# Kernel tuning notes

Hardware: AMD Instinct MI355X
Metric: run time of the kernel (lower is better)

The kernel has to match this reference:

```python
import jax, jax.numpy as jnp
import numpy as np

N_NODES = 100000
N_EDGES = 1600000
IN_CH = 128
TYPE_EMB = 32
OUT_CH = 128
N_REL = 8
N_BASES = 8
N_NTYPES = 8
FEAT = IN_CH + TYPE_EMB  # 160, RGCNConv input dim after concat


def setup_inputs() -> dict:
    key = jax.random.key(0)
    ks = jax.random.split(key, 9)
    x = jax.random.normal(ks[0], (N_NODES, IN_CH), dtype=jnp.float32)
    node_type_ids = jax.random.randint(ks[1], (N_NODES,), 0, N_NTYPES)
    edge_index = jax.random.randint(ks[2], (2, N_EDGES), 0, N_NODES)
    edge_type = jax.random.randint(ks[3], (N_EDGES,), 0, N_REL)
    emb_table = jax.random.normal(ks[4], (N_NTYPES, TYPE_EMB), dtype=jnp.float32)
    bases = jax.random.normal(ks[5], (N_BASES, FEAT, OUT_CH), dtype=jnp.float32) * (1.0 / np.sqrt(FEAT))
    comp = jax.random.normal(ks[6], (N_REL, N_BASES), dtype=jnp.float32) * (1.0 / np.sqrt(N_BASES))
    root_w = jax.random.normal(ks[7], (FEAT, OUT_CH), dtype=jnp.float32) * (1.0 / np.sqrt(FEAT))
    bias = jnp.zeros((OUT_CH,), dtype=jnp.float32)
    return {"x": x, "node_type_ids": node_type_ids, "edge_index": edge_index,
            "edge_type": edge_type, "emb_table": emb_table, "bases": bases,
            "comp": comp, "root_w": root_w, "bias": bias}


def reference(x, node_type_ids, edge_index, edge_type, emb_table, bases, comp, root_w, bias):
    N = x.shape[0]
    # node-type embedding lookup + concat
    h = jnp.concatenate([x, emb_table[node_type_ids]], axis=1)  # [N, FEAT]
    # basis decomposition: per-relation weights [R, FEAT, OUT]
    weight = jnp.einsum('rb,bio->rio', comp, bases)
    src, dst = edge_index[0], edge_index[1]
    h_src = h[src]  # [E, FEAT] -- dominant gather
    # root/self transform + bias
    out = h @ root_w + bias
    # PyG RGCNConv default aggr='mean': per-relation mean over incoming edges, summed across relations
    for r in range(weight.shape[0]):
        m = (edge_type == r).astype(h.dtype)  # [E]
        s = jax.ops.segment_sum(h_src * m[:, None], dst, num_segments=N)  # [N, FEAT]
        c = jax.ops.segment_sum(m, dst, num_segments=N)                    # [N]
        mean_r = s / jnp.maximum(c, 1.0)[:, None]
        out = out + mean_r @ weight[r]
    # dropout is identity in eval mode
    return jax.nn.relu(out)
```

## Files before the change

kernel.cpp:

```cpp
#include <hip/hip_runtime.h>

#define NN 100000
#define NE 1600000
#define INC 128
#define TE 32
#define OC 128
#define NR 8
#define NBASES 8
#define FT 160
#define KP 168
#define KW 160
#define TN 32
#define NBKT 3125
#define NCH 256
#define EPB 6250
#define CAP 896

typedef float f32x4 __attribute__((ext_vector_type(4)));
typedef float f32x2 __attribute__((ext_vector_type(2)));
typedef __bf16 bf16x8 __attribute__((ext_vector_type(8)));

__device__ __forceinline__ unsigned f2bf1(float f) {
    unsigned u = __float_as_uint(f);
    return (u + 0x7fffu + ((u >> 16) & 1u)) >> 16;
}

__device__ __forceinline__ float bflo(unsigned u) { return __uint_as_float(u << 16); }
__device__ __forceinline__ float bfhi(unsigned u) { return __uint_as_float(u & 0xFFFF0000u); }

__device__ __forceinline__ unsigned cvtpk(float a, float b) {
    unsigned r;
    asm("v_cvt_pk_bf16_f32 %0, %1, %2" : "=v"(r) : "v"(a), "v"(b));
    return r;
}

__device__ __forceinline__ int bscan_excl(int v, int* tmp) {
    int tid = threadIdx.x;
    tmp[tid] = v; __syncthreads();
#pragma unroll
    for (int d = 1; d < 256; d <<= 1) {
        int t = (tid >= d) ? tmp[tid - d] : 0;
        __syncthreads();
        tmp[tid] += t;
        __syncthreads();
    }
    return tmp[tid] - v;
}

__global__ __launch_bounds__(256) void k_prep(
    const float* __restrict__ x, const int* __restrict__ nt,
    const float* __restrict__ emb, const float* __restrict__ comp,
    const float* __restrict__ bases, const float* __restrict__ rootw,
    const int* __restrict__ ei,
    unsigned short* __restrict__ h, unsigned short* __restrict__ Wt,
    int* __restrict__ ghist, int* __restrict__ total) {
    __shared__ int hist[NBKT];
    int tid = threadIdx.x;
    int b = blockIdx.x;
    if (b < NCH) {
        for (int j = tid; j < NBKT; j += 256) hist[j] = 0;
        __syncthreads();
        int e0 = b * EPB;
#pragma unroll
        for (int kk = 0; kk < 28; kk += 4) {
            int dv[4];
#pragma unroll
            for (int u = 0; u < 4; u++) {
                int i = (kk + u) * 256 + tid;
                dv[u] = (i < EPB) ? ei[NE + e0 + i] : -1;
            }
#pragma unroll
            for (int u = 0; u < 4; u++)
                if (dv[u] >= 0) atomicAdd(&hist[dv[u] >> 5], 1);
        }
        __syncthreads();
        int* g = ghist + (size_t)b * NBKT;
        for (int j = tid; j < NBKT; j += 256) {
            int v = hist[j];
            g[j] = v;
            if (v) atomicAdd(&total[j], v);
        }
        return;
    }
    int idx = (b - NCH) * 256 + tid;
    if (idx < 9 * 128 * KW) {
        int ridx = idx / (128 * KW);
        int rem  = idx % (128 * KW);
        int o = rem / KW;
        int k = rem % KW;
        float v = 0.f;
        if (k < 128) {
            if (ridx < NR) {
#pragma unroll
                for (int bb = 0; bb < NBASES; bb++)
                    v += comp[ridx * NBASES + bb] * bases[(bb * FT + k) * OC + o];
            } else {
                v = rootw[k * OC + o];
            }
        } else if (k < 136) {
            int t = k - 128;
            if (ridx < NR) {
#pragma unroll
                for (int bb = 0; bb < NBASES; bb++) {
                    float cb = comp[ridx * NBASES + bb], s2 = 0.f;
                    for (int k2 = 0; k2 < TE; k2++)
                        s2 += emb[t * TE + k2] * bases[(bb * FT + 128 + k2) * OC + o];
                    v += cb * s2;
                }
            } else {
                for (int k2 = 0; k2 < TE; k2++)
                    v += emb[t * TE + k2] * rootw[(128 + k2) * OC + o];
            }
        }
        Wt[idx] = (unsigned short)f2bf1(v);
    }
    if (idx < NN * 16) {
        int n = idx / 16, c = idx % 16;
        const float* p = x + (size_t)n * INC + c * 8;
        f32x4 v0 = *(const f32x4*)p, v1 = *(const f32x4*)(p + 4);
        uint4 o;
        o.x = f2bf1(v0.x) | (f2bf1(v0.y) << 16);
        o.y = f2bf1(v0.z) | (f2bf1(v0.w) << 16);
        o.z = f2bf1(v1.x) | (f2bf1(v1.y) << 16);
        o.w = f2bf1(v1.z) | (f2bf1(v1.w) << 16);
        *(uint4*)(h + (size_t)n * INC + c * 8) = o;
    }
}

__global__ __launch_bounds__(256) void k_scanoff(const int* __restrict__ total,
                                                 int* __restrict__ ghist,
                                                 int* __restrict__ bstart) {
    __shared__ int tot[NBKT];
    __shared__ int tmp[256];
    int tid = threadIdx.x;
    for (int j = tid; j < NBKT; j += 256) tot[j] = total[j];
    __syncthreads();
    int i0 = tid * 13, s = 0;
    int loc[13];
#pragma unroll
    for (int i = 0; i < 13; i++) {
        int j = i0 + i;
        loc[i] = (j < NBKT) ? tot[j] : 0;
        s += loc[i];
    }
    int run = bscan_excl(s, tmp);
#pragma unroll
    for (int i = 0; i < 13; i++) {
        int j = i0 + i;
        if (j < NBKT) tot[j] = run;
        run += loc[i];
    }
    __syncthreads();
    if (blockIdx.x == 0) {
        for (int j = tid; j < NBKT; j += 256) bstart[j] = tot[j];
        if (tid == 0) bstart[NBKT] = NE;
    }
    int j = blockIdx.x * 256 + tid;
    if (j < NBKT) {
        int run2 = tot[j];
#pragma unroll 8
        for (int b = 0; b < NCH; b++) {
            int v = ghist[(size_t)b * NBKT + j];
            ghist[(size_t)b * NBKT + j] = run2;
            run2 += v;
        }
    }
}

__global__ __launch_bounds__(256) void k_scatter(const int* __restrict__ ei, const int* __restrict__ et,
                                                 const int* __restrict__ nt,
                                                 const int* __restrict__ ghist, unsigned* __restrict__ slots) {
    __shared__ int cur[NBKT];
    int tid = threadIdx.x, b = blockIdx.x;
    for (int j = tid; j < NBKT; j += 256) cur[j] = ghist[(size_t)b * NBKT + j];
    __syncthreads();
    int e0 = b * EPB;
#pragma unroll
    for (int kk = 0; kk < 28; kk += 4) {
        int sv[4], dv[4], rv[4], tv[4];
#pragma unroll
        for (int u = 0; u < 4; u++) {
            int i = (kk + u) * 256 + tid;
            int e = e0 + ((i < EPB) ? i : 0);
            sv[u] = ei[e]; dv[u] = ei[NE + e]; rv[u] = et[e];
            if (i >= EPB) dv[u] = -1;
        }
#pragma unroll
        for (int u = 0; u < 4; u++) tv[u] = nt[sv[u]];
#pragma unroll
        for (int u = 0; u < 4; u++) {
            if (dv[u] >= 0) {
                int pos = atomicAdd(&cur[dv[u] >> 5], 1);
                slots[pos] = (unsigned)sv[u] | ((unsigned)rv[u] << 17)
                           | ((unsigned)(dv[u] & 31) << 20) | ((unsigned)tv[u] << 25);
            }
        }
    }
}

__global__ __launch_bounds__(256, 6) void k_mega(
    const unsigned short* __restrict__ h, const int* __restrict__ nt,
    const float* __restrict__ bias,
    const unsigned short* __restrict__ Wt, const int* __restrict__ bstart,
    const unsigned* __restrict__ slots, float* __restrict__ out) {
    __shared__ unsigned short featmem[2][TN * KP];
    __shared__ unsigned sl[CAP];
    __shared__ unsigned pkl[256];

    const int tid = threadIdx.x;
    const int lane = tid & 63;
    const int wave = tid >> 6;
    const int j = blockIdx.x;
    const int n0 = j * TN;

    unsigned* sl_in = reinterpret_cast<unsigned*>(&featmem[0][0]);
    int* hist = reinterpret_cast<int*>(&featmem[0][0]) + CAP;
    int* tmp  = reinterpret_cast<int*>(&featmem[0][0]) + CAP + 256;

    int s0 = bstart[j];
    int m = bstart[j + 1] - s0; if (m > CAP) m = CAP;
    for (int i = tid; i < m; i += 256) sl_in[i] = slots[s0 + i];
    hist[tid] = 0;
    __syncthreads();
    for (int i = tid; i < m; i += 256) {
        unsigned v = sl_in[i];
        atomicAdd(&hist[((v >> 17) & 7u) * 32u + ((v >> 20) & 31u)], 1);
    }
    __syncthreads();
    int v0 = hist[tid];
    int ex = bscan_excl(v0, tmp);
    pkl[tid] = (unsigned)ex | ((unsigned)v0 << 16);
    hist[tid] = ex;
    __syncthreads();
    for (int i = tid; i < m; i += 256) {
        unsigned v = sl_in[i];
        int p = atomicAdd(&hist[((v >> 17) & 7u) * 32u + ((v >> 20) & 31u)], 1);
        sl[p] = (v & 0x1FFFFu) | (((v >> 25) & 7u) << 17);
    }
    __syncthreads();

    for (int i = tid; i < TN * 20; i += 256) {
        int nl = i / 20, c = i % 20, n = n0 + nl;
        uint4 v;
        if (c < 16) {
            v = *reinterpret_cast<const uint4*>(h + (size_t)n * INC + c * 8);
        } else if (c == 16) {
            int t = nt[n];
            v.x = (t == 0 ? 0x3F80u : 0u) | (t == 1 ? 0x3F800000u : 0u);
            v.y = (t == 2 ? 0x3F80u : 0u) | (t == 3 ? 0x3F800000u : 0u);
            v.z = (t == 4 ? 0x3F80u : 0u) | (t == 5 ? 0x3F800000u : 0u);
            v.w = (t == 6 ? 0x3F80u : 0u) | (t == 7 ? 0x3F800000u : 0u);
        } else {
            v = (uint4){0u, 0u, 0u, 0u};
        }
        *reinterpret_cast<uint4*>(&featmem[0][nl * KP + c * 8]) = v;
    }

    f32x4 acc[4];
#pragma unroll
    for (int t = 0; t < 4; t++) acc[t] = (f32x4){0.f, 0.f, 0.f, 0.f};

    auto mfma_pass = [&](int ridx, const unsigned short* fm) {
        const unsigned short* fA = fm + (lane & 15) * KP + ((lane >> 4) * 8);
        const unsigned short* gB = Wt + (size_t)ridx * 128 * KW
                                   + (wave * 32 + (lane & 15)) * KW + ((lane >> 4) * 8);
#pragma unroll
        for (int kc = 0; kc < 5; kc++) {
            bf16x8 a0 = *reinterpret_cast<const bf16x8*>(fA + 0 * 16 * KP + kc * 32);
            bf16x8 a1 = *reinterpret_cast<const bf16x8*>(fA + 1 * 16 * KP + kc * 32);
#pragma unroll
            for (int ct = 0; ct < 2; ct++) {
                bf16x8 b = *reinterpret_cast<const bf16x8*>(gB + ct * 16 * KW + kc * 32);
                acc[0 * 2 + ct] = __builtin_amdgcn_mfma_f32_16x16x32_bf16(a0, b, acc[0 * 2 + ct], 0, 0, 0);
                acc[1 * 2 + ct] = __builtin_amdgcn_mfma_f32_16x16x32_bf16(a1, b, acc[1 * 2 + ct], 0, 0, 0);
            }
        }
    };

    const int g = tid >> 4, l = tid & 15;
    const unsigned* hw = reinterpret_cast<const unsigned*>(h);

    auto agg_pass = [&](int r, unsigned short* fm) {
        int b0 = r * 32 + 2 * g;
        unsigned pk0 = pkl[b0], pk1 = pkl[b0 + 1];
        int sbeg = (int)(pk0 & 0xffffu);
        int e1 = (int)(pk1 & 0xffffu);
        int send = e1 + (int)(pk1 >> 16);
        f32x2 sa[4];
#pragma unroll
        for (int i = 0; i < 4; i++) sa[i] = (f32x2){0.f, 0.f};
        f32x2 cnt2 = (f32x2){0.f, 0.f};
        float run = 0.f;
        for (int e = sbeg; e < send; e += 4) {
            uint2 wa[4], wb[4]; unsigned tpk = 0;
#pragma unroll
            for (int u = 0; u < 4; u++) {
                int eu = e + u; if (eu >= send) eu = send - 1;
                unsigned v = sl[eu];
                const unsigned* hp = hw + (size_t)(v & 0x1FFFFu) * 64 + 2 * l;
                wa[u] = *reinterpret_cast<const uint2*>(hp);
                wb[u] = *reinterpret_cast<const uint2*>(hp + 32);
                tpk |= ((v >> 17) & 7u) << (3 * u);
            }
#pragma unroll
            for (int u = 0; u < 4; u++) {
                if (e + u < send) {
                    sa[0] += (f32x2){bflo(wa[u].x), bfhi(wa[u].x)};
                    sa[1] += (f32x2){bflo(wa[u].y), bfhi(wa[u].y)};
                    sa[2] += (f32x2){bflo(wb[u].x), bfhi(wb[u].x)};
                    sa[3] += (f32x2){bflo(wb[u].y), bfhi(wb[u].y)};
                    int tt = (int)((tpk >> (3 * u)) & 7u);
                    cnt2.x += (tt == 2 * l)     ? 1.f : 0.f;
                    cnt2.y += (tt == 2 * l + 1) ? 1.f : 0.f;
                    run += 1.f;
                    int nx = e + u + 1;
                    if (nx == e1 || nx == send) {
                        int q = (e + u >= e1) ? 1 : 0;
                        float inv = __builtin_amdgcn_rcpf(run);
                        f32x2 m0 = sa[0] * inv, m1 = sa[1] * inv, m2 = sa[2] * inv,
                              m3 = sa[3] * inv, fr = cnt2 * inv;
                        unsigned* fp = reinterpret_cast<unsigned*>(fm + (2 * g + q) * KP);
                        uint2 oa, ob;
                        oa.x = cvtpk(m0.x, m0.y);
                        oa.y = cvtpk(m1.x, m1.y);
                        ob.x = cvtpk(m2.x, m2.y);
                        ob.y = cvtpk(m3.x, m3.y);
                        *reinterpret_cast<uint2*>(fp + 2 * l) = oa;
                        *reinterpret_cast<uint2*>(fp + 32 + 2 * l) = ob;
                        fp[64 + l] = cvtpk(fr.x, fr.y);
#pragma unroll
                        for (int i = 0; i < 4; i++) sa[i] = (f32x2){0.f, 0.f};
                        cnt2 = (f32x2){0.f, 0.f};
                        run = 0.f;
                    }
                }
            }
        }
#pragma unroll
        for (int q = 0; q < 2; q++) {
            if ((pkl[b0 + q] >> 16) == 0u) {
                unsigned* fp = reinterpret_cast<unsigned*>(fm + (2 * g + q) * KP);
                *reinterpret_cast<uint2*>(fp + 2 * l) = (uint2){0u, 0u};
                *reinterpret_cast<uint2*>(fp + 32 + 2 * l) = (uint2){0u, 0u};
                fp[64 + l] = 0u;
            }
        }
    };

    __syncthreads();
    int prev = 8;
    for (int r = 0; r < NR; r++) {
        agg_pass(r, &featmem[(r + 1) & 1][0]);
        mfma_pass(prev, &featmem[r & 1][0]);
        prev = r;
        __syncthreads();
    }
    mfma_pass(7, &featmem[0][0]);

    const int rq = lane >> 4;
#pragma unroll
    for (int ct = 0; ct < 2; ct++) {
        int col = wave * 32 + ct * 16 + (lane & 15);
        float bv = bias[col];
#pragma unroll
        for (int rt = 0; rt < 2; rt++) {
#pragma unroll
            for (int i = 0; i < 4; i++) {
                int n = n0 + rt * 16 + rq * 4 + i;
                float v = acc[rt * 2 + ct][i] + bv;
                out[(size_t)n * OC + col] = v > 0.f ? v : 0.f;
            }
        }
    }
}

extern "C" void kernel_launch(void* const* d_in, const int* in_sizes, int n_in,
                              void* d_out, int out_size, void* d_ws, size_t ws_size,
                              hipStream_t stream) {
    const float* x     = (const float*)d_in[0];
    const int*   ntype = (const int*)d_in[1];
    const int*   ei    = (const int*)d_in[2];
    const int*   et    = (const int*)d_in[3];
    const float* emb   = (const float*)d_in[4];
    const float* bases = (const float*)d_in[5];
    const float* comp  = (const float*)d_in[6];
    const float* rootw = (const float*)d_in[7];
    const float* bias  = (const float*)d_in[8];
    float* out = (float*)d_out;

    char* ws = (char*)d_ws;
    unsigned short* Wt     = (unsigned short*)(ws);
    unsigned short* h      = (unsigned short*)(ws + 368640);
    int*            ghist  = (int*)(ws + 25968640);
    int*            total  = (int*)(ws + 29168640);
    int*            bstart = (int*)(ws + 29181184);
    unsigned*       slots  = (unsigned*)(ws + 29193728);

    hipMemsetAsync(total, 0, NBKT * sizeof(int), stream);
    k_prep   <<<NCH + 6250, 256, 0, stream>>>(x, ntype, emb, comp, bases, rootw, ei, h, Wt, ghist, total);
    k_scanoff<<<13,   256, 0, stream>>>(total, ghist, bstart);
    k_scatter<<<NCH,  256, 0, stream>>>(ei, et, ntype, ghist, slots);
    k_mega   <<<NBKT, 256, 0, stream>>>(h, ntype, bias, Wt, bstart, slots, out);
}
```

Baseline: 339.8 us.

## Process 64-node buckets per block in two 32-node halves with MFMA priority

Doubles the destination bucket size to 64 nodes, so edge sorting, per-block histogramming and the local scan handle two sub-tiles that the main kernel walks as two sequential 32-node halves reusing the same LDS feature buffers. This halves the number of buckets and blocks, which spreads the per-block setup cost (slot load, histogram, scan) over more nodes and cuts the ghist scan work. It also raises the wave priority around the MFMA section. The cost is more LDS for slots and histogram, a lower occupancy hint (5 instead of 6), and a serial dependency between the two halves inside one block.

```diff
diff --git a/kernel.cpp b/kernel.cpp
--- a/kernel.cpp
+++ b/kernel.cpp
@@ -10,11 +10,11 @@
 #define FT 160
 #define KP 168
 #define KW 160
-#define TN 32
-#define NBKT 3125
+#define TN 64
+#define NBKT 1563
 #define NCH 256
 #define EPB 6250
-#define CAP 896
+#define CAP 1536
 
 typedef float f32x4 __attribute__((ext_vector_type(4)));
 typedef float f32x2 __attribute__((ext_vector_type(2)));
@@ -71,7 +71,7 @@
             }
 #pragma unroll
             for (int u = 0; u < 4; u++)
-                if (dv[u] >= 0) atomicAdd(&hist[dv[u] >> 5], 1);
+                if (dv[u] >= 0) atomicAdd(&hist[dv[u] >> 6], 1);
         }
         __syncthreads();
         int* g = ghist + (size_t)b * NBKT;
@@ -135,17 +135,17 @@
     int tid = threadIdx.x;
     for (int j = tid; j < NBKT; j += 256) tot[j] = total[j];
     __syncthreads();
-    int i0 = tid * 13, s = 0;
-    int loc[13];
-#pragma unroll
-    for (int i = 0; i < 13; i++) {
+    int i0 = tid * 7, s = 0;
+    int loc[7];
+#pragma unroll
+    for (int i = 0; i < 7; i++) {
         int j = i0 + i;
         loc[i] = (j < NBKT) ? tot[j] : 0;
         s += loc[i];
     }
     int run = bscan_excl(s, tmp);
 #pragma unroll
-    for (int i = 0; i < 13; i++) {
+    for (int i = 0; i < 7; i++) {
         int j = i0 + i;
         if (j < NBKT) tot[j] = run;
         run += loc[i];
@@ -190,22 +190,22 @@
 #pragma unroll
         for (int u = 0; u < 4; u++) {
             if (dv[u] >= 0) {
-                int pos = atomicAdd(&cur[dv[u] >> 5], 1);
+                int pos = atomicAdd(&cur[dv[u] >> 6], 1);
                 slots[pos] = (unsigned)sv[u] | ((unsigned)rv[u] << 17)
-                           | ((unsigned)(dv[u] & 31) << 20) | ((unsigned)tv[u] << 25);
-            }
-        }
-    }
-}
-
-__global__ __launch_bounds__(256, 6) void k_mega(
+                           | ((unsigned)(dv[u] & 63) << 20) | ((unsigned)tv[u] << 26);
+            }
+        }
+    }
+}
+
+__global__ __launch_bounds__(256, 5) void k_mega(
     const unsigned short* __restrict__ h, const int* __restrict__ nt,
     const float* __restrict__ bias,
     const unsigned short* __restrict__ Wt, const int* __restrict__ bstart,
     const unsigned* __restrict__ slots, float* __restrict__ out) {
-    __shared__ unsigned short featmem[2][TN * KP];
+    __shared__ unsigned short featmem[2][32 * KP];
     __shared__ unsigned sl[CAP];
-    __shared__ unsigned pkl[256];
+    __shared__ unsigned pkl[512];
 
     const int tid = threadIdx.x;
     const int lane = tid & 63;
@@ -215,55 +215,37 @@
 
     unsigned* sl_in = reinterpret_cast<unsigned*>(&featmem[0][0]);
     int* hist = reinterpret_cast<int*>(&featmem[0][0]) + CAP;
-    int* tmp  = reinterpret_cast<int*>(&featmem[0][0]) + CAP + 256;
+    int* tmp  = reinterpret_cast<int*>(&featmem[0][0]) + CAP + 512;
 
     int s0 = bstart[j];
     int m = bstart[j + 1] - s0; if (m > CAP) m = CAP;
     for (int i = tid; i < m; i += 256) sl_in[i] = slots[s0 + i];
-    hist[tid] = 0;
+    hist[2 * tid] = 0; hist[2 * tid + 1] = 0;
     __syncthreads();
     for (int i = tid; i < m; i += 256) {
         unsigned v = sl_in[i];
-        atomicAdd(&hist[((v >> 17) & 7u) * 32u + ((v >> 20) & 31u)], 1);
-    }
-    __syncthreads();
-    int v0 = hist[tid];
-    int ex = bscan_excl(v0, tmp);
-    pkl[tid] = (unsigned)ex | ((unsigned)v0 << 16);
-    hist[tid] = ex;
+        atomicAdd(&hist[((v >> 17) & 7u) * 64u + ((v >> 20) & 63u)], 1);
+    }
+    __syncthreads();
+    int v0 = hist[2 * tid], v1 = hist[2 * tid + 1];
+    int ex = bscan_excl(v0 + v1, tmp);
+    pkl[2 * tid]     = (unsigned)ex | ((unsigned)v0 << 16);
+    pkl[2 * tid + 1] = (unsigned)(ex + v0) | ((unsigned)v1 << 16);
+    hist[2 * tid] = ex; hist[2 * tid + 1] = ex + v0;
     __syncthreads();
     for (int i = tid; i < m; i += 256) {
         unsigned v = sl_in[i];
-        int p = atomicAdd(&hist[((v >> 17) & 7u) * 32u + ((v >> 20) & 31u)], 1);
-        sl[p] = (v & 0x1FFFFu) | (((v >> 25) & 7u) << 17);
-    }
-    __syncthreads();
-
-    for (int i = tid; i < TN * 20; i += 256) {
-        int nl = i / 20, c = i % 20, n = n0 + nl;
-        uint4 v;
-        if (c < 16) {
-            v = *reinterpret_cast<const uint4*>(h + (size_t)n * INC + c * 8);
-        } else if (c == 16) {
-            int t = nt[n];
-            v.x = (t == 0 ? 0x3F80u : 0u) | (t == 1 ? 0x3F800000u : 0u);
-            v.y = (t == 2 ? 0x3F80u : 0u) | (t == 3 ? 0x3F800000u : 0u);
-            v.z = (t == 4 ? 0x3F80u : 0u) | (t == 5 ? 0x3F800000u : 0u);
-            v.w = (t == 6 ? 0x3F80u : 0u) | (t == 7 ? 0x3F800000u : 0u);
-        } else {
-            v = (uint4){0u, 0u, 0u, 0u};
-        }
-        *reinterpret_cast<uint4*>(&featmem[0][nl * KP + c * 8]) = v;
+        int p = atomicAdd(&hist[((v >> 17) & 7u) * 64u + ((v >> 20) & 63u)], 1);
+        sl[p] = (v & 0x1FFFFu) | (((v >> 26) & 7u) << 17);
     }
 
     f32x4 acc[4];
-#pragma unroll
-    for (int t = 0; t < 4; t++) acc[t] = (f32x4){0.f, 0.f, 0.f, 0.f};
 
     auto mfma_pass = [&](int ridx, const unsigned short* fm) {
         const unsigned short* fA = fm + (lane & 15) * KP + ((lane >> 4) * 8);
         const unsigned short* gB = Wt + (size_t)ridx * 128 * KW
                                    + (wave * 32 + (lane & 15)) * KW + ((lane >> 4) * 8);
+        __builtin_amdgcn_s_setprio(1);
 #pragma unroll
         for (int kc = 0; kc < 5; kc++) {
             bf16x8 a0 = *reinterpret_cast<const bf16x8*>(fA + 0 * 16 * KP + kc * 32);
@@ -275,13 +257,14 @@
                 acc[1 * 2 + ct] = __builtin_amdgcn_mfma_f32_16x16x32_bf16(a1, b, acc[1 * 2 + ct], 0, 0, 0);
             }
         }
+        __builtin_amdgcn_s_setprio(0);
     };
 
     const int g = tid >> 4, l = tid & 15;
     const unsigned* hw = reinterpret_cast<const unsigned*>(h);
 
-    auto agg_pass = [&](int r, unsigned short* fm) {
-        int b0 = r * 32 + 2 * g;
+    auto agg_pass = [&](int r, int t, unsigned short* fm) {
+        int b0 = r * 64 + t * 32 + 2 * g;
         unsigned pk0 = pkl[b0], pk1 = pkl[b0 + 1];
         int sbeg = (int)(pk0 & 0xffffu);
         int e1 = (int)(pk1 & 0xffffu);
@@ -347,28 +330,53 @@
         }
     };
 
-    __syncthreads();
-    int prev = 8;
-    for (int r = 0; r < NR; r++) {
-        agg_pass(r, &featmem[(r + 1) & 1][0]);
-        mfma_pass(prev, &featmem[r & 1][0]);
-        prev = r;
-        __syncthreads();
-    }
-    mfma_pass(7, &featmem[0][0]);
-
     const int rq = lane >> 4;
-#pragma unroll
-    for (int ct = 0; ct < 2; ct++) {
-        int col = wave * 32 + ct * 16 + (lane & 15);
-        float bv = bias[col];
-#pragma unroll
-        for (int rt = 0; rt < 2; rt++) {
-#pragma unroll
-            for (int i = 0; i < 4; i++) {
-                int n = n0 + rt * 16 + rq * 4 + i;
-                float v = acc[rt * 2 + ct][i] + bv;
-                out[(size_t)n * OC + col] = v > 0.f ? v : 0.f;
+    for (int t = 0; t < 2; t++) {
+        __syncthreads();
+
+        for (int i = tid; i < 32 * 20; i += 256) {
+            int nl = i / 20, c = i % 20, n = n0 + t * 32 + nl;
+            uint4 v;
+            if (c < 16) {
+                v = *reinterpret_cast<const uint4*>(h + (size_t)n * INC + c * 8);
+            } else if (c == 16) {
+                int tt = (n < NN) ? nt[n] : 0;
+                v.x = (tt == 0 ? 0x3F80u : 0u) | (tt == 1 ? 0x3F800000u : 0u);
+                v.y = (tt == 2 ? 0x3F80u : 0u) | (tt == 3 ? 0x3F800000u : 0u);
+                v.z = (tt == 4 ? 0x3F80u : 0u) | (tt == 5 ? 0x3F800000u : 0u);
+                v.w = (tt == 6 ? 0x3F80u : 0u) | (tt == 7 ? 0x3F800000u : 0u);
+            } else {
+                v = (uint4){0u, 0u, 0u, 0u};
+            }
+            *reinterpret_cast<uint4*>(&featmem[0][nl * KP + c * 8]) = v;
+        }
+#pragma unroll
+        for (int q = 0; q < 4; q++) acc[q] = (f32x4){0.f, 0.f, 0.f, 0.f};
+        __syncthreads();
+
+        int prev = 8;
+        for (int r = 0; r < NR; r++) {
+            agg_pass(r, t, &featmem[(r + 1) & 1][0]);
+            mfma_pass(prev, &featmem[r & 1][0]);
+            prev = r;
+            __syncthreads();
+        }
+        mfma_pass(7, &featmem[0][0]);
+
+#pragma unroll
+        for (int ct = 0; ct < 2; ct++) {
+            int col = wave * 32 + ct * 16 + (lane & 15);
+            float bv = bias[col];
+#pragma unroll
+            for (int rt = 0; rt < 2; rt++) {
+#pragma unroll
+                for (int i = 0; i < 4; i++) {
+                    int n = n0 + t * 32 + rt * 16 + rq * 4 + i;
+                    if (n < NN) {
+                        float v = acc[rt * 2 + ct][i] + bv;
+                        out[(size_t)n * OC + col] = v > 0.f ? v : 0.f;
+                    }
+                }
             }
         }
     }
@@ -392,13 +400,13 @@
     unsigned short* Wt     = (unsigned short*)(ws);
     unsigned short* h      = (unsigned short*)(ws + 368640);
     int*            ghist  = (int*)(ws + 25968640);
-    int*            total  = (int*)(ws + 29168640);
-    int*            bstart = (int*)(ws + 29181184);
-    unsigned*       slots  = (unsigned*)(ws + 29193728);
+    int*            total  = (int*)(ws + 27569152);
+    int*            bstart = (int*)(ws + 27575552);
+    unsigned*       slots  = (unsigned*)(ws + 27581952);
 
     hipMemsetAsync(total, 0, NBKT * sizeof(int), stream);
     k_prep   <<<NCH + 6250, 256, 0, stream>>>(x, ntype, emb, comp, bases, rootw, ei, h, Wt, ghist, total);
-    k_scanoff<<<13,   256, 0, stream>>>(total, ghist, bstart);
+    k_scanoff<<<7,    256, 0, stream>>>(total, ghist, bstart);
     k_scatter<<<NCH,  256, 0, stream>>>(ei, et, ntype, ghist, slots);
     k_mega   <<<NBKT, 256, 0, stream>>>(h, ntype, bias, Wt, bstart, slots, out);
 }
```

Result: slower. 369.9 us (+8.9%).
